# Kernel optimization log

Hardware: AMD Instinct MI355X
Metric: run time of the kernel (lower is better)

The kernel has to match this reference:

```python
import jax, jax.numpy as jnp
import numpy as np

N_AFFINES = 4
N_SDFS = 4
BATCH = 8192
DEPTH = 6


def setup_inputs() -> dict:
    key = jax.random.key(0)
    k1, k2, k3, k4, k5, k6, k7 = jax.random.split(key, 7)
    query = jax.random.normal(k1, (BATCH, 2), dtype=jnp.float32)
    # Contractive affines: scale*rotation + translation (homogeneous 3x3), guaranteed invertible.
    theta = jax.random.uniform(k2, (N_AFFINES,), minval=0.0, maxval=2.0 * np.pi)
    s = 0.4 + 0.2 * jax.random.uniform(k3, (N_AFFINES,))  # contraction factors in [0.4, 0.6]
    t = 0.4 * jax.random.normal(k4, (N_AFFINES, 2))
    c, sn = jnp.cos(theta), jnp.sin(theta)
    row0 = jnp.stack([s * c, -s * sn, t[:, 0]], axis=-1)
    row1 = jnp.stack([s * sn, s * c, t[:, 1]], axis=-1)
    row2 = jnp.broadcast_to(jnp.array([0.0, 0.0, 1.0]), (N_AFFINES, 3))
    affine_mats = jnp.stack([row0, row1, row2], axis=1).astype(jnp.float32)  # (N,3,3)
    sdf_centers = 0.5 * jax.random.normal(k5, (N_SDFS, 2), dtype=jnp.float32)
    sdf_radii = (0.3 + 0.2 * jax.random.uniform(k6, (N_SDFS,))).astype(jnp.float32)
    return {
        "query": query,
        "affine_scales": s.astype(jnp.float32),
        "affine_mats": affine_mats,
        "sdf_centers": sdf_centers,
        "sdf_radii": sdf_radii,
        "depth": DEPTH,
    }


def reference(query, affine_scales, affine_mats, sdf_centers, sdf_radii, depth):
    # back transforms: inverse matrices and reciprocal scales
    back_scales = 1.0 / affine_scales              # (N,)
    back_mats = jnp.linalg.inv(affine_mats)        # (N,3,3)

    # Compose all N^depth transform combinations (mirrors the nested list comprehension).
    Tm = jnp.eye(3, dtype=jnp.float32)[None]       # (1,3,3)
    sc = jnp.ones((1,), dtype=jnp.float32)         # (1,)
    for _ in range(depth):
        Tm = jnp.einsum('aij,njk->anik', Tm, back_mats).reshape(-1, 3, 3)
        sc = (sc[:, None] * back_scales[None, :]).reshape(-1)
    # Tm: (T,3,3), sc: (T,) with T = N^depth

    B = query.shape[0]
    qpad = jnp.concatenate([query, jnp.ones((B, 1), dtype=query.dtype)], axis=1)  # (B,3)
    qt = jnp.einsum('tij,bj->tbi', Tm, qpad)[..., :2]  # (T,B,2)

    # Circle SDFs: ||p - center|| - radius, batched over all K sdfs -> (T,K,B)
    diff = qt[:, None, :, :] - sdf_centers[None, :, None, :]
    d = jnp.sqrt(jnp.sum(diff * diff, axis=-1)) - sdf_radii[None, :, None]
    d = d / sc[:, None, None]  # 1/scale * sdf(...)

    return jnp.min(jnp.min(d, axis=0), axis=0)  # (B,)
```

## Files before the change

kernel.cpp:

```cpp
#include <hip/hip_runtime.h>
#include <math.h>


#define NA 4
#define T_TOTAL 4096
#define BATCH 8192
#define TPB 256
#define TCHUNK 64
#define NCHUNK 64
#define PPL 4

__device__ __forceinline__ float fsqrt(float x) { return __builtin_amdgcn_sqrtf(x); }

__constant__ unsigned char LO_COMBO[64] = {
    0, 21, 42, 63,
    1, 4, 16,   2, 8, 32,   3, 12, 48,
    20, 17, 5,  22, 25, 37, 23, 29, 53,
    40, 34, 10, 41, 38, 26, 43, 46, 58,
    60, 51, 15, 61, 55, 31, 62, 59, 47,
    6, 9, 18, 24, 33, 36,
    7, 13, 19, 28, 49, 52,
    11, 14, 35, 44, 50, 56,
    27, 30, 39, 45, 54, 57
};


__device__ __forceinline__ void compute_inverses(const float* __restrict__ mats,
                                                 const float* __restrict__ scales,
                                                 float (*inv)[8], int tid) {
    if (tid < NA) {
        const int n = tid;
        float a = mats[n * 9 + 0], b = mats[n * 9 + 1], e = mats[n * 9 + 2];
        float c = mats[n * 9 + 3], d = mats[n * 9 + 4], f = mats[n * 9 + 5];
        float rd = 1.0f / (a * d - b * c);
        float i00 = d * rd, i01 = -b * rd, i10 = -c * rd, i11 = a * rd;
        inv[n][0] = i00; inv[n][1] = i01; inv[n][2] = i10; inv[n][3] = i11;
        inv[n][4] = -(i00 * e + i01 * f);
        inv[n][5] = -(i10 * e + i11 * f);
        inv[n][6] = scales[n];
        inv[n][7] = 0.0f;
    }
}

__device__ __forceinline__ void gen_transforms(const float (*inv)[8], float4 (*xf)[4],
                                               int hi, int tid, int nthreads,
                                               const float* __restrict__ centers,
                                               const float* __restrict__ radii) {
    for (int i = tid; i < TCHUNK; i += nthreads) {
        int t = hi * 64 + (int)LO_COMBO[i];
        int dg = (t >> 10) & 3;
        float m00 = inv[dg][0], m01 = inv[dg][1], m10 = inv[dg][2], m11 = inv[dg][3];
        float tx = inv[dg][4], ty = inv[dg][5], sp = inv[dg][6];
        #pragma unroll
        for (int s = 8; s >= 0; s -= 2) {
            dg = (t >> s) & 3;
            float b00 = inv[dg][0], b01 = inv[dg][1], b10 = inv[dg][2], b11 = inv[dg][3];
            float bx = inv[dg][4], by = inv[dg][5];
            float n00 = fmaf(m00, b00, m01 * b10);
            float n01 = fmaf(m00, b01, m01 * b11);
            float n10 = fmaf(m10, b00, m11 * b10);
            float n11 = fmaf(m10, b01, m11 * b11);
            float nx  = fmaf(m00, bx, fmaf(m01, by, tx));
            float ny  = fmaf(m10, bx, fmaf(m11, by, ty));
            m00 = n00; m01 = n01; m10 = n10; m11 = n11; tx = nx; ty = ny;
            sp *= inv[dg][6];
        }
        float R00 = m00 * sp, R01 = m01 * sp, R10 = m10 * sp, R11 = m11 * sp;
        #pragma unroll
        for (int k = 0; k < 4; ++k) {
            float ex = (tx - centers[2 * k + 0]) * sp;
            float ey = (ty - centers[2 * k + 1]) * sp;
            float wx = 2.0f * fmaf(R00, ex, R10 * ey);
            float wy = 2.0f * fmaf(R01, ex, R11 * ey);
            float ee = fmaf(ex, ex, ey * ey);
            xf[i][k] = make_float4(wx, wy, ee, radii[k] * sp);
        }
    }
}

template <int SZ>
__device__ __forceinline__ void group_evalP(const float4 (*xf)[4], int slot,
                                            const float* qx, const float* qy,
                                            const float* qq, float* d) {
    float sm[PPL][4];
    float rsp[4];
    #pragma unroll
    for (int k = 0; k < 4; ++k) {
        float4 W = xf[slot][k];
        rsp[k] = W.w;
        #pragma unroll
        for (int p = 0; p < PPL; ++p)
            sm[p][k] = fmaf(W.x, qx[p], fmaf(W.y, qy[p], W.z));
    }
    #pragma unroll
    for (int i = 1; i < SZ; ++i) {
        #pragma unroll
        for (int k = 0; k < 4; ++k) {
            float4 W = xf[slot + i][k];
            #pragma unroll
            for (int p = 0; p < PPL; ++p)
                sm[p][k] = fminf(sm[p][k], fmaf(W.x, qx[p], fmaf(W.y, qy[p], W.z)));
        }
    }
    #pragma unroll
    for (int p = 0; p < PPL; ++p) {
        #pragma unroll
        for (int k = 0; k < 4; ++k)
            d[p] = fminf(d[p], fsqrt(fmaxf(sm[p][k] + qq[p], 0.0f)) - rsp[k]);
    }
}

__device__ __forceinline__ void accum_groupedP(const float4 (*xf)[4],
                                               const float* qx, const float* qy,
                                               const float* qq, float* d) {
    #pragma unroll 1
    for (int a = 0; a < 4; ++a)
        group_evalP<1>(xf, a, qx, qy, qq, d);
    #pragma unroll 1
    for (int m = 0; m < 12; ++m)
        group_evalP<3>(xf, 4 + 3 * m, qx, qy, qq, d);
    #pragma unroll 1
    for (int g = 0; g < 4; ++g)
        group_evalP<6>(xf, 40 + 6 * g, qx, qy, qq, d);
}


__global__ __launch_bounds__(TPB) void ifs_partial4(const float* __restrict__ query,
                                                    const float* __restrict__ scales,
                                                    const float* __restrict__ mats,
                                                    const float* __restrict__ centers,
                                                    const float* __restrict__ radii,
                                                    float* __restrict__ partial) {
    __shared__ float inv[NA][8];
    __shared__ float4 xf[TCHUNK][4];
    const int tid = threadIdx.x;

    compute_inverses(mats, scales, inv, tid);
    __syncthreads();

    gen_transforms(inv, xf, blockIdx.y, tid, TPB, centers, radii);
    __syncthreads();

    const int base = blockIdx.x * (PPL * TPB) + tid;
    const float2* q2 = (const float2*)query;

    float qx[PPL], qy[PPL], qq[PPL], d[PPL];
    #pragma unroll
    for (int p = 0; p < PPL; ++p) {
        float2 q = q2[base + p * TPB];
        qx[p] = q.x; qy[p] = q.y;
        qq[p] = fmaf(q.x, q.x, q.y * q.y);
        d[p] = INFINITY;
    }

    accum_groupedP(xf, qx, qy, qq, d);

    float* prow = partial + blockIdx.y * BATCH + base;
    #pragma unroll
    for (int p = 0; p < PPL; ++p) prow[p * TPB] = d[p];
}

__global__ __launch_bounds__(256) void ifs_reduce(const float* __restrict__ partial,
                                                  float* __restrict__ out) {
    const int b = blockIdx.x * 256 + threadIdx.x;
    float m = INFINITY;
    #pragma unroll
    for (int c = 0; c < NCHUNK; ++c) m = fminf(m, partial[c * BATCH + b]);
    out[b] = m;
}

__global__ __launch_bounds__(256) void ifs_mono(const float* __restrict__ query,
                                                const float* __restrict__ scales,
                                                const float* __restrict__ mats,
                                                const float* __restrict__ centers,
                                                const float* __restrict__ radii,
                                                float* __restrict__ out) {
    __shared__ float inv[NA][8];
    __shared__ float4 xf[TCHUNK][4];
    const int tid = threadIdx.x;

    compute_inverses(mats, scales, inv, tid);
    __syncthreads();

    const int pb = blockIdx.x * 256 + tid;
    float4 qv = ((const float4*)query)[pb];
    float qx[2] = {qv.x, qv.z}, qy[2] = {qv.y, qv.w};
    float qq[2] = {fmaf(qv.x, qv.x, qv.y * qv.y), fmaf(qv.z, qv.z, qv.w * qv.w)};
    float d[2] = {INFINITY, INFINITY};

    for (int hi = 0; hi < NCHUNK; ++hi) {
        __syncthreads();
        gen_transforms(inv, xf, hi, tid, 256, centers, radii);
        __syncthreads();
        float sm[2][4], rsp[4];
        #pragma unroll 1
        for (int a = 0; a < 4; ++a) {
            #pragma unroll
            for (int k = 0; k < 4; ++k) {
                float4 W = xf[a][k]; rsp[k] = W.w;
                #pragma unroll
                for (int p = 0; p < 2; ++p)
                    sm[p][k] = fmaf(W.x, qx[p], fmaf(W.y, qy[p], W.z));
            }
            #pragma unroll
            for (int p = 0; p < 2; ++p)
                #pragma unroll
                for (int k = 0; k < 4; ++k)
                    d[p] = fminf(d[p], fsqrt(fmaxf(sm[p][k] + qq[p], 0.0f)) - rsp[k]);
        }
        #pragma unroll 1
        for (int m = 0; m < 12; ++m) {
            int slot = 4 + 3 * m;
            #pragma unroll
            for (int k = 0; k < 4; ++k) {
                float4 W = xf[slot][k]; rsp[k] = W.w;
                #pragma unroll
                for (int p = 0; p < 2; ++p)
                    sm[p][k] = fmaf(W.x, qx[p], fmaf(W.y, qy[p], W.z));
            }
            #pragma unroll
            for (int i = 1; i < 3; ++i)
                #pragma unroll
                for (int k = 0; k < 4; ++k) {
                    float4 W = xf[slot + i][k];
                    #pragma unroll
                    for (int p = 0; p < 2; ++p)
                        sm[p][k] = fminf(sm[p][k], fmaf(W.x, qx[p], fmaf(W.y, qy[p], W.z)));
                }
            #pragma unroll
            for (int p = 0; p < 2; ++p)
                #pragma unroll
                for (int k = 0; k < 4; ++k)
                    d[p] = fminf(d[p], fsqrt(fmaxf(sm[p][k] + qq[p], 0.0f)) - rsp[k]);
        }
        #pragma unroll 1
        for (int g = 0; g < 4; ++g) {
            int slot = 40 + 6 * g;
            #pragma unroll
            for (int k = 0; k < 4; ++k) {
                float4 W = xf[slot][k]; rsp[k] = W.w;
                #pragma unroll
                for (int p = 0; p < 2; ++p)
                    sm[p][k] = fmaf(W.x, qx[p], fmaf(W.y, qy[p], W.z));
            }
            #pragma unroll
            for (int i = 1; i < 6; ++i)
                #pragma unroll
                for (int k = 0; k < 4; ++k) {
                    float4 W = xf[slot + i][k];
                    #pragma unroll
                    for (int p = 0; p < 2; ++p)
                        sm[p][k] = fminf(sm[p][k], fmaf(W.x, qx[p], fmaf(W.y, qy[p], W.z)));
                }
            #pragma unroll
            for (int p = 0; p < 2; ++p)
                #pragma unroll
                for (int k = 0; k < 4; ++k)
                    d[p] = fminf(d[p], fsqrt(fmaxf(sm[p][k] + qq[p], 0.0f)) - rsp[k]);
        }
    }
    ((float2*)out)[pb] = make_float2(d[0], d[1]);
}


extern "C" void kernel_launch(void* const* d_in, const int* in_sizes, int n_in,
                              void* d_out, int out_size, void* d_ws, size_t ws_size,
                              hipStream_t stream) {
    const float* query   = (const float*)d_in[0];
    const float* scales  = (const float*)d_in[1];
    const float* mats    = (const float*)d_in[2];
    const float* centers = (const float*)d_in[3];
    const float* radii   = (const float*)d_in[4];
    float* out = (float*)d_out;

    const size_t needed = (size_t)NCHUNK * BATCH * sizeof(float);

    if (ws_size >= needed) {
        float* partial = (float*)d_ws;
        dim3 grid(BATCH / (TPB * PPL), NCHUNK);
        ifs_partial4<<<grid, TPB, 0, stream>>>(query, scales, mats, centers,
                                               radii, partial);
        ifs_reduce<<<BATCH / 256, 256, 0, stream>>>(partial, out);
    } else {
        ifs_mono<<<BATCH / (256 * 2), 256, 0, stream>>>(query, scales, mats, centers,
                                                        radii, out);
    }
}
```

Measured before the change: 80.71 us.

## Precompute transform table in separate kernel, read it from global in eval kernel

Moves per-chunk transform generation out of the partial-eval kernel into a dedicated ifs_gen kernel that writes all 4096x4 transform coefficients to workspace once. The eval kernel then reads its coefficients directly from global memory (cached, uniform across the block) instead of recomputing them per block and synchronising through shared memory. This removes redundant recomputation across the 8 x-blocks sharing each chunk and two barriers, at the cost of an extra kernel launch and global-memory reads in the inner loop. The fallback mono kernel's grouped loops are merged into one dynamic-size loop.

```diff
diff --git a/kernel.cpp b/kernel.cpp
--- a/kernel.cpp
+++ b/kernel.cpp
@@ -42,51 +42,59 @@
     }
 }
 
-__device__ __forceinline__ void gen_transforms(const float (*inv)[8], float4 (*xf)[4],
-                                               int hi, int tid, int nthreads,
+__global__ __launch_bounds__(TPB) void ifs_gen(const float* __restrict__ scales,
+                                               const float* __restrict__ mats,
                                                const float* __restrict__ centers,
-                                               const float* __restrict__ radii) {
-    for (int i = tid; i < TCHUNK; i += nthreads) {
-        int t = hi * 64 + (int)LO_COMBO[i];
-        int dg = (t >> 10) & 3;
-        float m00 = inv[dg][0], m01 = inv[dg][1], m10 = inv[dg][2], m11 = inv[dg][3];
-        float tx = inv[dg][4], ty = inv[dg][5], sp = inv[dg][6];
-        #pragma unroll
-        for (int s = 8; s >= 0; s -= 2) {
-            dg = (t >> s) & 3;
-            float b00 = inv[dg][0], b01 = inv[dg][1], b10 = inv[dg][2], b11 = inv[dg][3];
-            float bx = inv[dg][4], by = inv[dg][5];
-            float n00 = fmaf(m00, b00, m01 * b10);
-            float n01 = fmaf(m00, b01, m01 * b11);
-            float n10 = fmaf(m10, b00, m11 * b10);
-            float n11 = fmaf(m10, b01, m11 * b11);
-            float nx  = fmaf(m00, bx, fmaf(m01, by, tx));
-            float ny  = fmaf(m10, bx, fmaf(m11, by, ty));
-            m00 = n00; m01 = n01; m10 = n10; m11 = n11; tx = nx; ty = ny;
-            sp *= inv[dg][6];
-        }
-        float R00 = m00 * sp, R01 = m01 * sp, R10 = m10 * sp, R11 = m11 * sp;
-        #pragma unroll
-        for (int k = 0; k < 4; ++k) {
-            float ex = (tx - centers[2 * k + 0]) * sp;
-            float ey = (ty - centers[2 * k + 1]) * sp;
-            float wx = 2.0f * fmaf(R00, ex, R10 * ey);
-            float wy = 2.0f * fmaf(R01, ex, R11 * ey);
-            float ee = fmaf(ex, ex, ey * ey);
-            xf[i][k] = make_float4(wx, wy, ee, radii[k] * sp);
-        }
-    }
-}
+                                               const float* __restrict__ radii,
+                                               float4* __restrict__ xfg) {
+    __shared__ float inv[NA][8];
+    const int tid = threadIdx.x;
+    compute_inverses(mats, scales, inv, tid);
+    __syncthreads();
+
+    const int g = blockIdx.x * TPB + tid;
+    const int hi = g >> 6;
+    const int t = hi * 64 + (int)LO_COMBO[g & 63];
+
+    int dg = (t >> 10) & 3;
+    float m00 = inv[dg][0], m01 = inv[dg][1], m10 = inv[dg][2], m11 = inv[dg][3];
+    float tx = inv[dg][4], ty = inv[dg][5], sp = inv[dg][6];
+    #pragma unroll
+    for (int s = 8; s >= 0; s -= 2) {
+        dg = (t >> s) & 3;
+        float b00 = inv[dg][0], b01 = inv[dg][1], b10 = inv[dg][2], b11 = inv[dg][3];
+        float bx = inv[dg][4], by = inv[dg][5];
+        float n00 = fmaf(m00, b00, m01 * b10);
+        float n01 = fmaf(m00, b01, m01 * b11);
+        float n10 = fmaf(m10, b00, m11 * b10);
+        float n11 = fmaf(m10, b01, m11 * b11);
+        float nx  = fmaf(m00, bx, fmaf(m01, by, tx));
+        float ny  = fmaf(m10, bx, fmaf(m11, by, ty));
+        m00 = n00; m01 = n01; m10 = n10; m11 = n11; tx = nx; ty = ny;
+        sp *= inv[dg][6];
+    }
+    float R00 = m00 * sp, R01 = m01 * sp, R10 = m10 * sp, R11 = m11 * sp;
+    #pragma unroll
+    for (int k = 0; k < 4; ++k) {
+        float ex = (tx - centers[2 * k + 0]) * sp;
+        float ey = (ty - centers[2 * k + 1]) * sp;
+        float wx = 2.0f * fmaf(R00, ex, R10 * ey);
+        float wy = 2.0f * fmaf(R01, ex, R11 * ey);
+        float ee = fmaf(ex, ex, ey * ey);
+        xfg[g * 4 + k] = make_float4(wx, wy, ee, radii[k] * sp);
+    }
+}
+
 
 template <int SZ>
-__device__ __forceinline__ void group_evalP(const float4 (*xf)[4], int slot,
+__device__ __forceinline__ void group_evalP(const float4* __restrict__ xf, int slot,
                                             const float* qx, const float* qy,
                                             const float* qq, float* d) {
     float sm[PPL][4];
     float rsp[4];
     #pragma unroll
     for (int k = 0; k < 4; ++k) {
-        float4 W = xf[slot][k];
+        float4 W = xf[slot * 4 + k];
         rsp[k] = W.w;
         #pragma unroll
         for (int p = 0; p < PPL; ++p)
@@ -96,7 +104,7 @@
     for (int i = 1; i < SZ; ++i) {
         #pragma unroll
         for (int k = 0; k < 4; ++k) {
-            float4 W = xf[slot + i][k];
+            float4 W = xf[(slot + i) * 4 + k];
             #pragma unroll
             for (int p = 0; p < PPL; ++p)
                 sm[p][k] = fminf(sm[p][k], fmaf(W.x, qx[p], fmaf(W.y, qy[p], W.z)));
@@ -110,9 +118,24 @@
     }
 }
 
-__device__ __forceinline__ void accum_groupedP(const float4 (*xf)[4],
-                                               const float* qx, const float* qy,
-                                               const float* qq, float* d) {
+__global__ __launch_bounds__(TPB) void ifs_eval(const float* __restrict__ query,
+                                                const float4* __restrict__ xfg,
+                                                float* __restrict__ partial) {
+    const float4* __restrict__ xf = xfg + (size_t)blockIdx.y * TCHUNK * 4;
+
+    const int tid = threadIdx.x;
+    const int base = blockIdx.x * (PPL * TPB) + tid;
+    const float2* q2 = (const float2*)query;
+
+    float qx[PPL], qy[PPL], qq[PPL], d[PPL];
+    #pragma unroll
+    for (int p = 0; p < PPL; ++p) {
+        float2 q = q2[base + p * TPB];
+        qx[p] = q.x; qy[p] = q.y;
+        qq[p] = fmaf(q.x, q.x, q.y * q.y);
+        d[p] = INFINITY;
+    }
+
     #pragma unroll 1
     for (int a = 0; a < 4; ++a)
         group_evalP<1>(xf, a, qx, qy, qq, d);
@@ -122,38 +145,6 @@
     #pragma unroll 1
     for (int g = 0; g < 4; ++g)
         group_evalP<6>(xf, 40 + 6 * g, qx, qy, qq, d);
-}
-
-
-__global__ __launch_bounds__(TPB) void ifs_partial4(const float* __restrict__ query,
-                                                    const float* __restrict__ scales,
-                                                    const float* __restrict__ mats,
-                                                    const float* __restrict__ centers,
-                                                    const float* __restrict__ radii,
-                                                    float* __restrict__ partial) {
-    __shared__ float inv[NA][8];
-    __shared__ float4 xf[TCHUNK][4];
-    const int tid = threadIdx.x;
-
-    compute_inverses(mats, scales, inv, tid);
-    __syncthreads();
-
-    gen_transforms(inv, xf, blockIdx.y, tid, TPB, centers, radii);
-    __syncthreads();
-
-    const int base = blockIdx.x * (PPL * TPB) + tid;
-    const float2* q2 = (const float2*)query;
-
-    float qx[PPL], qy[PPL], qq[PPL], d[PPL];
-    #pragma unroll
-    for (int p = 0; p < PPL; ++p) {
-        float2 q = q2[base + p * TPB];
-        qx[p] = q.x; qy[p] = q.y;
-        qq[p] = fmaf(q.x, q.x, q.y * q.y);
-        d[p] = INFINITY;
-    }
-
-    accum_groupedP(xf, qx, qy, qq, d);
 
     float* prow = partial + blockIdx.y * BATCH + base;
     #pragma unroll
@@ -176,7 +167,7 @@
                                                 const float* __restrict__ radii,
                                                 float* __restrict__ out) {
     __shared__ float inv[NA][8];
-    __shared__ float4 xf[TCHUNK][4];
+    __shared__ float4 xfs[TCHUNK][4];
     const int tid = threadIdx.x;
 
     compute_inverses(mats, scales, inv, tid);
@@ -190,73 +181,62 @@
 
     for (int hi = 0; hi < NCHUNK; ++hi) {
         __syncthreads();
-        gen_transforms(inv, xf, hi, tid, 256, centers, radii);
+        for (int i = tid; i < TCHUNK; i += 256) {
+            int t = hi * 64 + (int)LO_COMBO[i];
+            int dg = (t >> 10) & 3;
+            float m00 = inv[dg][0], m01 = inv[dg][1], m10 = inv[dg][2], m11 = inv[dg][3];
+            float tx = inv[dg][4], ty = inv[dg][5], sp = inv[dg][6];
+            #pragma unroll
+            for (int s = 8; s >= 0; s -= 2) {
+                dg = (t >> s) & 3;
+                float b00 = inv[dg][0], b01 = inv[dg][1], b10 = inv[dg][2], b11 = inv[dg][3];
+                float bx = inv[dg][4], by = inv[dg][5];
+                float n00 = fmaf(m00, b00, m01 * b10);
+                float n01 = fmaf(m00, b01, m01 * b11);
+                float n10 = fmaf(m10, b00, m11 * b10);
+                float n11 = fmaf(m10, b01, m11 * b11);
+                float nx  = fmaf(m00, bx, fmaf(m01, by, tx));
+                float ny  = fmaf(m10, bx, fmaf(m11, by, ty));
+                m00 = n00; m01 = n01; m10 = n10; m11 = n11; tx = nx; ty = ny;
+                sp *= inv[dg][6];
+            }
+            float R00 = m00 * sp, R01 = m01 * sp, R10 = m10 * sp, R11 = m11 * sp;
+            #pragma unroll
+            for (int k = 0; k < 4; ++k) {
+                float ex = (tx - centers[2 * k + 0]) * sp;
+                float ey = (ty - centers[2 * k + 1]) * sp;
+                float wx = 2.0f * fmaf(R00, ex, R10 * ey);
+                float wy = 2.0f * fmaf(R01, ex, R11 * ey);
+                float ee = fmaf(ex, ex, ey * ey);
+                xfs[i][k] = make_float4(wx, wy, ee, radii[k] * sp);
+            }
+        }
         __syncthreads();
         float sm[2][4], rsp[4];
         #pragma unroll 1
-        for (int a = 0; a < 4; ++a) {
+        for (int slot0 = 0; slot0 < 64; ) {
+            int sz = (slot0 < 4) ? 1 : (slot0 < 40 ? 3 : 6);
             #pragma unroll
             for (int k = 0; k < 4; ++k) {
-                float4 W = xf[a][k]; rsp[k] = W.w;
+                float4 W = xfs[slot0][k]; rsp[k] = W.w;
                 #pragma unroll
                 for (int p = 0; p < 2; ++p)
                     sm[p][k] = fmaf(W.x, qx[p], fmaf(W.y, qy[p], W.z));
             }
+            for (int i = 1; i < sz; ++i)
+                #pragma unroll
+                for (int k = 0; k < 4; ++k) {
+                    float4 W = xfs[slot0 + i][k];
+                    #pragma unroll
+                    for (int p = 0; p < 2; ++p)
+                        sm[p][k] = fminf(sm[p][k], fmaf(W.x, qx[p], fmaf(W.y, qy[p], W.z)));
+                }
             #pragma unroll
             for (int p = 0; p < 2; ++p)
                 #pragma unroll
                 for (int k = 0; k < 4; ++k)
                     d[p] = fminf(d[p], fsqrt(fmaxf(sm[p][k] + qq[p], 0.0f)) - rsp[k]);
-        }
-        #pragma unroll 1
-        for (int m = 0; m < 12; ++m) {
-            int slot = 4 + 3 * m;
-            #pragma unroll
-            for (int k = 0; k < 4; ++k) {
-                float4 W = xf[slot][k]; rsp[k] = W.w;
-                #pragma unroll
-                for (int p = 0; p < 2; ++p)
-                    sm[p][k] = fmaf(W.x, qx[p], fmaf(W.y, qy[p], W.z));
-            }
-            #pragma unroll
-            for (int i = 1; i < 3; ++i)
-                #pragma unroll
-                for (int k = 0; k < 4; ++k) {
-                    float4 W = xf[slot + i][k];
-                    #pragma unroll
-                    for (int p = 0; p < 2; ++p)
-                        sm[p][k] = fminf(sm[p][k], fmaf(W.x, qx[p], fmaf(W.y, qy[p], W.z)));
-                }
-            #pragma unroll
-            for (int p = 0; p < 2; ++p)
-                #pragma unroll
-                for (int k = 0; k < 4; ++k)
-                    d[p] = fminf(d[p], fsqrt(fmaxf(sm[p][k] + qq[p], 0.0f)) - rsp[k]);
-        }
-        #pragma unroll 1
-        for (int g = 0; g < 4; ++g) {
-            int slot = 40 + 6 * g;
-            #pragma unroll
-            for (int k = 0; k < 4; ++k) {
-                float4 W = xf[slot][k]; rsp[k] = W.w;
-                #pragma unroll
-                for (int p = 0; p < 2; ++p)
-                    sm[p][k] = fmaf(W.x, qx[p], fmaf(W.y, qy[p], W.z));
-            }
-            #pragma unroll
-            for (int i = 1; i < 6; ++i)
-                #pragma unroll
-                for (int k = 0; k < 4; ++k) {
-                    float4 W = xf[slot + i][k];
-                    #pragma unroll
-                    for (int p = 0; p < 2; ++p)
-                        sm[p][k] = fminf(sm[p][k], fmaf(W.x, qx[p], fmaf(W.y, qy[p], W.z)));
-                }
-            #pragma unroll
-            for (int p = 0; p < 2; ++p)
-                #pragma unroll
-                for (int k = 0; k < 4; ++k)
-                    d[p] = fminf(d[p], fsqrt(fmaxf(sm[p][k] + qq[p], 0.0f)) - rsp[k]);
+            slot0 += sz;
         }
     }
     ((float2*)out)[pb] = make_float2(d[0], d[1]);
@@ -273,13 +253,15 @@
     const float* radii   = (const float*)d_in[4];
     float* out = (float*)d_out;
 
-    const size_t needed = (size_t)NCHUNK * BATCH * sizeof(float);
+    const size_t xfg_bytes = (size_t)T_TOTAL * 4 * sizeof(float4);
+    const size_t needed = xfg_bytes + (size_t)NCHUNK * BATCH * sizeof(float);
 
     if (ws_size >= needed) {
-        float* partial = (float*)d_ws;
+        float4* xfg    = (float4*)d_ws;
+        float* partial = (float*)((char*)d_ws + xfg_bytes);
+        ifs_gen<<<T_TOTAL / TPB, TPB, 0, stream>>>(scales, mats, centers, radii, xfg);
         dim3 grid(BATCH / (TPB * PPL), NCHUNK);
-        ifs_partial4<<<grid, TPB, 0, stream>>>(query, scales, mats, centers,
-                                               radii, partial);
+        ifs_eval<<<grid, TPB, 0, stream>>>(query, xfg, partial);
         ifs_reduce<<<BATCH / 256, 256, 0, stream>>>(partial, out);
     } else {
         ifs_mono<<<BATCH / (256 * 2), 256, 0, stream>>>(query, scales, mats, centers,
```

Result: slower. 87.37 us (+8.2%).
